# Optimization experiments

Measured on AMD Instinct MI355X. Metric: run time of the kernel, lower is better.

## Reference

```python
import jax, jax.numpy as jnp
import numpy as np

N, E, DIM = 50000, 500000, 64
EIN3, EIN4 = 16, 16

def setup_inputs() -> dict:
    key = jax.random.key(0)
    ks = jax.random.split(key, 8)
    x = jax.random.normal(ks[0], (N, DIM), dtype=jnp.float32)
    edge_index3 = jax.random.randint(ks[1], (2, E), 0, N, dtype=jnp.int64)
    edge_attr3 = jax.random.normal(ks[2], (E, EIN3), dtype=jnp.float32)
    edge_attr4 = jax.random.normal(ks[3], (E, EIN4), dtype=jnp.float32)
    batch = jnp.zeros((N,), dtype=jnp.int64)
    # MLP params: Linear(2*dim, 4*dim) -> ReLU -> Linear(4*dim, 1)
    W1 = jax.random.normal(ks[4], (2 * DIM, 4 * DIM), dtype=jnp.float32) / np.sqrt(2 * DIM)
    b1 = jnp.zeros((4 * DIM,), dtype=jnp.float32)
    W2 = jax.random.normal(ks[5], (4 * DIM, 1), dtype=jnp.float32) / np.sqrt(4 * DIM)
    b2 = jnp.zeros((1,), dtype=jnp.float32)
    return {"x": x, "edge_index3": edge_index3, "edge_attr3": edge_attr3,
            "edge_attr4": edge_attr4, "batch": batch,
            "W1": W1, "b1": b1, "W2": W2, "b2": b2}

def reference(x, edge_index3, edge_attr3, edge_attr4, batch, W1, b1, W2, b2):
    # gather endpoints: temp[k] = x[edge_index3[k]] -> [E, dim]
    src = x[edge_index3[0]]  # [E, dim]
    dst = x[edge_index3[1]]  # [E, dim]
    # symmetric concat: [[src|dst], [dst|src]] -> [2E, 2*dim]
    yhat = jnp.concatenate([
        jnp.concatenate([src, dst], axis=1),
        jnp.concatenate([dst, src], axis=1)], axis=0)
    h = jax.nn.relu(yhat @ W1 + b1)        # [2E, 4*dim]
    y = (h @ W2 + b2)[:, 0]                # [2E]
    return y.reshape(2, -1).mean(axis=0)   # [E]
```

## Files before the change

### kernel.cpp

```cpp
#include <hip/hip_runtime.h>

#define DIM 64
#define HID 256
#define ROWB 512
#define QSCALE  25.4f
#define DQSCALE (5.0f/127.0f)

typedef short s8v  __attribute__((ext_vector_type(8)));
typedef float f4v  __attribute__((ext_vector_type(4)));
typedef float f2v  __attribute__((ext_vector_type(2)));
typedef unsigned short u16x2 __attribute__((ext_vector_type(2)));

union U16 { uint4 u; s8v s; };

__device__ __forceinline__ unsigned short bf16_rne(float f) {
    unsigned u = __float_as_uint(f);
    u = (u + 0x7fffu + ((u >> 16) & 1u)) >> 16;
    return (unsigned short)u;
}
__device__ __forceinline__ unsigned pk_bf16(float a, float b) {
    return (unsigned)bf16_rne(a) | ((unsigned)bf16_rne(b) << 16);
}

__device__ __forceinline__ u16x2 as_u16x2(unsigned v) { union { unsigned u; u16x2 s; } c; c.u = v; return c.s; }
__device__ __forceinline__ unsigned as_u32(u16x2 v)   { union { u16x2 s; unsigned u; } c; c.s = v; return c.u; }

#define DPP_ADD(x, ctrl, rmask)                                               \
    (x) += __int_as_float(__builtin_amdgcn_update_dpp(                        \
        0, __float_as_int(x), (ctrl), (rmask), 0xf, true))
#define DPP_REDUCE5(x) do {                                                   \
    DPP_ADD(x, 0x111, 0xf);                                                   \
    DPP_ADD(x, 0x112, 0xf);                                                   \
    DPP_ADD(x, 0x114, 0xf);                                                   \
    DPP_ADD(x, 0x118, 0xf);                                                   \
    DPP_ADD(x, 0x142, 0xa);                                                   \
} while (0)

__global__ __launch_bounds__(256) void prep_wfrag(
    const float* __restrict__ W1, unsigned short* __restrict__ wf)
{
    const int f = blockIdx.x * 256 + threadIdx.x;
    if (f >= 32 * 2 * 64) return;
    const int lane = f & 63;
    const int t    = (f >> 6) & 1;
    const int ct   = f >> 7;
    const int col  = ct * 16 + (lane & 15);
    const int k0   = t * 32 + (lane >> 4) * 8;
    const float* __restrict__ wsrc =
        W1 + ((col >= HID) ? (DIM * HID + col - HID) : col);
    unsigned short v[8];
#pragma unroll
    for (int j = 0; j < 8; ++j) v[j] = bf16_rne(wsrc[(size_t)(k0 + j) * HID]);
    uint4 o;
    o.x = (unsigned)v[0] | ((unsigned)v[1] << 16);
    o.y = (unsigned)v[2] | ((unsigned)v[3] << 16);
    o.z = (unsigned)v[4] | ((unsigned)v[5] << 16);
    o.w = (unsigned)v[6] | ((unsigned)v[7] << 16);
    *(uint4*)(wf + (size_t)f * 8) = o;
}

__global__ __launch_bounds__(256) void node_mfma_q(
    const float* __restrict__ x, const unsigned short* __restrict__ wf,
    const float* __restrict__ b1, unsigned char* __restrict__ tab, int n)
{
    const int lane    = threadIdx.x & 63;
    const int w       = threadIdx.x >> 6;
    const int rowgrp  = w >> 1;
    const int colhalf = w & 1;
    const int m       = lane & 15;
    const int quad    = lane >> 4;
    const int rbase   = blockIdx.x * 32 + rowgrp * 16;

    const int arow = rbase + m;
    const float* __restrict__ xr = x + (size_t)((arow < n) ? arow : (n - 1)) * DIM;
    s8v a[2];
#pragma unroll
    for (int t = 0; t < 2; ++t) {
        const float4 lo = *(const float4*)(xr + t * 32 + quad * 8);
        const float4 hi = *(const float4*)(xr + t * 32 + quad * 8 + 4);
        U16 u;
        u.u.x = pk_bf16(lo.x, lo.y);
        u.u.y = pk_bf16(lo.z, lo.w);
        u.u.z = pk_bf16(hi.x, hi.y);
        u.u.w = pk_bf16(hi.z, hi.w);
        a[t] = u.s;
    }

    const uint4* __restrict__ wfv = (const uint4*)wf;

    f4v acc[16];
#pragma unroll
    for (int ct = 0; ct < 16; ++ct) {
        const int ctg = colhalf * 16 + ct;
        U16 b0u, b1u;
        b0u.u = wfv[(ctg * 2 + 0) * 64 + lane];
        b1u.u = wfv[(ctg * 2 + 1) * 64 + lane];
        f4v c = {0.f, 0.f, 0.f, 0.f};
        c = __builtin_amdgcn_mfma_f32_16x16x32_bf16(a[0], b0u.s, c, 0, 0, 0);
        c = __builtin_amdgcn_mfma_f32_16x16x32_bf16(a[1], b1u.s, c, 0, 0, 0);
        if (colhalf == 0) {
            const float bias = b1[ctg * 16 + m];
            c[0] += bias; c[1] += bias; c[2] += bias; c[3] += bias;
        }
        acc[ct] = c;
    }

#pragma unroll
    for (int r = 0; r < 4; ++r) {
        const int gr = rbase + quad * 4 + r;
        if (gr >= n) continue;
        unsigned b[16];
#pragma unroll
        for (int ct = 0; ct < 16; ++ct) {
            float v = __builtin_rintf(acc[ct][r] * QSCALE);
            v = fminf(fmaxf(v, -127.f), 127.f);
            b[ct] = (unsigned)((int)v + 127);
        }
        uint4 o;
        o.x = b[0]  | (b[1]  << 8) | (b[2]  << 16) | (b[3]  << 24);
        o.y = b[4]  | (b[5]  << 8) | (b[6]  << 16) | (b[7]  << 24);
        o.z = b[8]  | (b[9]  << 8) | (b[10] << 16) | (b[11] << 24);
        o.w = b[12] | (b[13] << 8) | (b[14] << 16) | (b[15] << 24);
        *(uint4*)(tab + (size_t)gr * ROWB + colhalf * 256 + m * 16) = o;
    }
}

__device__ __forceinline__ float pass_dot(const uint4 S, const uint4 D,
                                          const f2v* __restrict__ w)
{
    const unsigned sa[4] = {S.x, S.y, S.z, S.w};
    const unsigned da[4] = {D.x, D.y, D.z, D.w};
    const u16x2 k254 = {254, 254};
    f2v acc; acc.x = 0.f; acc.y = 0.f;
#pragma unroll
    for (int i = 0; i < 4; ++i) {
        const unsigned zs0 = __builtin_amdgcn_perm(0u, sa[i], 0x0C010C00u);
        const unsigned zs1 = __builtin_amdgcn_perm(0u, sa[i], 0x0C030C02u);
        const unsigned zd0 = __builtin_amdgcn_perm(0u, da[i], 0x0C010C00u);
        const unsigned zd1 = __builtin_amdgcn_perm(0u, da[i], 0x0C030C02u);
        const unsigned r0 = as_u32(__builtin_elementwise_sub_sat(
                                as_u16x2(zs0) + as_u16x2(zd0), k254));
        const unsigned r1 = as_u32(__builtin_elementwise_sub_sat(
                                as_u16x2(zs1) + as_u16x2(zd1), k254));
        f2v f0, f1;
        f0.x = (float)(r0 & 0xffu);
        f0.y = (float)((r0 >> 16) & 0xffu);
        f1.x = (float)(r1 & 0xffu);
        f1.y = (float)((r1 >> 16) & 0xffu);
        acc = f0 * w[2 * i] + acc;
        acc = f1 * w[2 * i + 1] + acc;
    }
    return acc.x + acc.y;
}

__global__ __launch_bounds__(256, 8) void edge_mlp_q(
    const int* __restrict__ ei, const unsigned char* __restrict__ tab,
    const float* __restrict__ W2, const float* __restrict__ b2,
    float* __restrict__ out, int ne)
{
    const int lane = threadIdx.x & 63;
    const int l31  = lane & 31;
    const int m    = lane & 15;
    const bool hi  = lane >= 32;

    f2v w[8];
#pragma unroll
    for (int i = 0; i < 4; ++i) {
        f2v w0, w1;
        w0.x = W2[(4 * i + 0) * 16 + m]; w0.y = W2[(4 * i + 1) * 16 + m];
        w1.x = W2[(4 * i + 2) * 16 + m]; w1.y = W2[(4 * i + 3) * 16 + m];
        w[2 * i] = w0; w[2 * i + 1] = w1;
    }
    const float bias = b2[0];
    const float sc   = 0.5f * DQSCALE;

    const unsigned offS = 16u * (unsigned)l31;
    const unsigned offD = 16u * (unsigned)(l31 ^ 16);

    const int wid = blockIdx.x * 4 + (threadIdx.x >> 6);
    const int nw  = (int)gridDim.x * 4;
    const int ne4 = ne & ~3;

    for (int e0 = wid * 4; e0 < ne4; e0 += nw * 4) {
        const int eu = __builtin_amdgcn_readfirstlane(e0);
        const int s0 = ei[eu],          s1 = ei[eu + 1];
        const int s2 = ei[eu + 2],      s3 = ei[eu + 3];
        const int d0 = ei[ne + eu],     d1 = ei[ne + eu + 1];
        const int d2 = ei[ne + eu + 2], d3 = ei[ne + eu + 3];

        const uint4 T0 = *(const uint4*)(tab + (((unsigned)(hi ? s1 : s0)) << 9) + offS);
        const uint4 T1 = *(const uint4*)(tab + (((unsigned)(hi ? d1 : d0)) << 9) + offD);
        const uint4 T2 = *(const uint4*)(tab + (((unsigned)(hi ? s3 : s2)) << 9) + offS);
        const uint4 T3 = *(const uint4*)(tab + (((unsigned)(hi ? d3 : d2)) << 9) + offD);

        float r0 = pass_dot(T0, T1, w);
        DPP_REDUCE5(r0);
        float r1 = pass_dot(T2, T3, w);
        DPP_REDUCE5(r1);

        if (l31 == 31) {
            const int eo = eu + (lane >> 5);
            out[eo]     = fmaf(sc, r0, bias);
            out[eo + 2] = fmaf(sc, r1, bias);
        }
    }

    if ((ne & 3) && wid == 0) {
        for (int e = ne4; e < ne; ++e) {
            const int s = ei[e], d = ei[ne + e];
            const uint4 S = *(const uint4*)(tab + ((unsigned)s << 9) + offS);
            const uint4 D = *(const uint4*)(tab + ((unsigned)d << 9) + offD);
            float r = pass_dot(S, D, w);
            DPP_REDUCE5(r);
            if (lane == 31) out[e] = fmaf(sc, r, bias);
        }
    }
}

extern "C" void kernel_launch(void* const* d_in, const int* in_sizes, int n_in,
                              void* d_out, int out_size, void* d_ws, size_t ws_size,
                              hipStream_t stream) {
    const float* x  = (const float*)d_in[0];
    const int*   ei = (const int*)d_in[1];
    const float* W1 = (const float*)d_in[5];
    const float* b1 = (const float*)d_in[6];
    const float* W2 = (const float*)d_in[7];
    const float* b2 = (const float*)d_in[8];
    float* out = (float*)d_out;

    const int n  = in_sizes[0] / DIM;
    const int ne = in_sizes[1] / 2;

    unsigned char*  tab = (unsigned char*)d_ws;
    unsigned short* wf  = (unsigned short*)(tab + (size_t)n * ROWB);

    prep_wfrag<<<16, 256, 0, stream>>>(W1, wf);
    node_mfma_q<<<(n + 31) / 32, 256, 0, stream>>>(x, wf, b1, tab, n);
    edge_mlp_q<<<8192, 256, 0, stream>>>(ei, tab, W2, b2, out, ne);
}
```

Baseline: 187.3 us.

## Process one edge per full wave with 8-byte loads and 64-lane reduction

Each edge is now spread across all 64 lanes, with each lane loading 8 bytes instead of 16 from the precomputed quantized table. Before, each 32-lane half-wave handled a different edge. The wave issues 8 gathers for 4 edges and reduces each with a 6-step DPP sum across 64 lanes. One lane writes the 4 outputs as a single float4 store. The aim is smaller per-lane loads, fewer VGPRs and a vectorized store, at the cost of more cross-lane reduction steps and more load instructions.

New measurement: 186.6 us. About the same (-0.4%).

```diff
diff --git a/kernel.cpp b/kernel.cpp
--- a/kernel.cpp
+++ b/kernel.cpp
@@ -28,12 +28,13 @@
 #define DPP_ADD(x, ctrl, rmask)                                               \
     (x) += __int_as_float(__builtin_amdgcn_update_dpp(                        \
         0, __float_as_int(x), (ctrl), (rmask), 0xf, true))
-#define DPP_REDUCE5(x) do {                                                   \
-    DPP_ADD(x, 0x111, 0xf);                                                   \
-    DPP_ADD(x, 0x112, 0xf);                                                   \
-    DPP_ADD(x, 0x114, 0xf);                                                   \
-    DPP_ADD(x, 0x118, 0xf);                                                   \
-    DPP_ADD(x, 0x142, 0xa);                                                   \
+#define WAVE_SUM64(x) do {                                                    \
+    DPP_ADD(x, 0x111, 0xf);                                   \
+    DPP_ADD(x, 0x112, 0xf);                                   \
+    DPP_ADD(x, 0x114, 0xf);                                   \
+    DPP_ADD(x, 0x118, 0xf);                                   \
+    DPP_ADD(x, 0x142, 0xa);                                 \
+    DPP_ADD(x, 0x143, 0xc);               \
 } while (0)
 
 __global__ __launch_bounds__(256) void prep_wfrag(
@@ -125,31 +126,33 @@
     }
 }
 
-__device__ __forceinline__ float pass_dot(const uint4 S, const uint4 D,
+__device__ __forceinline__ void dot_dword(const unsigned s, const unsigned d,
+                                          const f2v wlo, const f2v whi, f2v& acc)
+{
+    const u16x2 k254 = {254, 254};
+    const unsigned zs0 = __builtin_amdgcn_perm(0u, s, 0x0C010C00u);
+    const unsigned zs1 = __builtin_amdgcn_perm(0u, s, 0x0C030C02u);
+    const unsigned zd0 = __builtin_amdgcn_perm(0u, d, 0x0C010C00u);
+    const unsigned zd1 = __builtin_amdgcn_perm(0u, d, 0x0C030C02u);
+    const unsigned r0 = as_u32(__builtin_elementwise_sub_sat(
+                            as_u16x2(zs0) + as_u16x2(zd0), k254));
+    const unsigned r1 = as_u32(__builtin_elementwise_sub_sat(
+                            as_u16x2(zs1) + as_u16x2(zd1), k254));
+    f2v f0, f1;
+    f0.x = (float)(r0 & 0xffu);
+    f0.y = (float)((r0 >> 16) & 0xffu);
+    f1.x = (float)(r1 & 0xffu);
+    f1.y = (float)((r1 >> 16) & 0xffu);
+    acc = f0 * wlo + acc;
+    acc = f1 * whi + acc;
+}
+
+__device__ __forceinline__ float pair_dot(const uint2 S, const uint2 D,
                                           const f2v* __restrict__ w)
 {
-    const unsigned sa[4] = {S.x, S.y, S.z, S.w};
-    const unsigned da[4] = {D.x, D.y, D.z, D.w};
-    const u16x2 k254 = {254, 254};
     f2v acc; acc.x = 0.f; acc.y = 0.f;
-#pragma unroll
-    for (int i = 0; i < 4; ++i) {
-        const unsigned zs0 = __builtin_amdgcn_perm(0u, sa[i], 0x0C010C00u);
-        const unsigned zs1 = __builtin_amdgcn_perm(0u, sa[i], 0x0C030C02u);
-        const unsigned zd0 = __builtin_amdgcn_perm(0u, da[i], 0x0C010C00u);
-        const unsigned zd1 = __builtin_amdgcn_perm(0u, da[i], 0x0C030C02u);
-        const unsigned r0 = as_u32(__builtin_elementwise_sub_sat(
-                                as_u16x2(zs0) + as_u16x2(zd0), k254));
-        const unsigned r1 = as_u32(__builtin_elementwise_sub_sat(
-                                as_u16x2(zs1) + as_u16x2(zd1), k254));
-        f2v f0, f1;
-        f0.x = (float)(r0 & 0xffu);
-        f0.y = (float)((r0 >> 16) & 0xffu);
-        f1.x = (float)(r1 & 0xffu);
-        f1.y = (float)((r1 >> 16) & 0xffu);
-        acc = f0 * w[2 * i] + acc;
-        acc = f1 * w[2 * i + 1] + acc;
-    }
+    dot_dword(S.x, D.x, w[0], w[1], acc);
+    dot_dword(S.y, D.y, w[2], w[3], acc);
     return acc.x + acc.y;
 }
 
@@ -159,23 +162,23 @@
     float* __restrict__ out, int ne)
 {
     const int lane = threadIdx.x & 63;
-    const int l31  = lane & 31;
-    const int m    = lane & 15;
-    const bool hi  = lane >= 32;
-
-    f2v w[8];
-#pragma unroll
-    for (int i = 0; i < 4; ++i) {
-        f2v w0, w1;
-        w0.x = W2[(4 * i + 0) * 16 + m]; w0.y = W2[(4 * i + 1) * 16 + m];
-        w1.x = W2[(4 * i + 2) * 16 + m]; w1.y = W2[(4 * i + 3) * 16 + m];
-        w[2 * i] = w0; w[2 * i + 1] = w1;
+    const int lp   = lane & 31;
+    const int mcol = lp >> 1;
+    const int ctb  = (lp & 1) * 8;
+
+    f2v w[4];
+#pragma unroll
+    for (int k = 0; k < 4; ++k) {
+        f2v t;
+        t.x = W2[(ctb + 2 * k)     * 16 + mcol];
+        t.y = W2[(ctb + 2 * k + 1) * 16 + mcol];
+        w[k] = t;
     }
     const float bias = b2[0];
     const float sc   = 0.5f * DQSCALE;
 
-    const unsigned offS = 16u * (unsigned)l31;
-    const unsigned offD = 16u * (unsigned)(l31 ^ 16);
+    const unsigned offS = 8u * (unsigned)lane;
+    const unsigned offD = 8u * (unsigned)(lane ^ 32);
 
     const int wid = blockIdx.x * 4 + (threadIdx.x >> 6);
     const int nw  = (int)gridDim.x * 4;
@@ -183,36 +186,36 @@
 
     for (int e0 = wid * 4; e0 < ne4; e0 += nw * 4) {
         const int eu = __builtin_amdgcn_readfirstlane(e0);
-        const int s0 = ei[eu],          s1 = ei[eu + 1];
-        const int s2 = ei[eu + 2],      s3 = ei[eu + 3];
-        const int d0 = ei[ne + eu],     d1 = ei[ne + eu + 1];
-        const int d2 = ei[ne + eu + 2], d3 = ei[ne + eu + 3];
-
-        const uint4 T0 = *(const uint4*)(tab + (((unsigned)(hi ? s1 : s0)) << 9) + offS);
-        const uint4 T1 = *(const uint4*)(tab + (((unsigned)(hi ? d1 : d0)) << 9) + offD);
-        const uint4 T2 = *(const uint4*)(tab + (((unsigned)(hi ? s3 : s2)) << 9) + offS);
-        const uint4 T3 = *(const uint4*)(tab + (((unsigned)(hi ? d3 : d2)) << 9) + offD);
-
-        float r0 = pass_dot(T0, T1, w);
-        DPP_REDUCE5(r0);
-        float r1 = pass_dot(T2, T3, w);
-        DPP_REDUCE5(r1);
-
-        if (l31 == 31) {
-            const int eo = eu + (lane >> 5);
-            out[eo]     = fmaf(sc, r0, bias);
-            out[eo + 2] = fmaf(sc, r1, bias);
+        uint2 hs[4], hd[4];
+#pragma unroll
+        for (int q = 0; q < 4; ++q) {
+            const int s = ei[eu + q];
+            const int d = ei[ne + eu + q];
+            hs[q] = *(const uint2*)(tab + ((size_t)(unsigned)s << 9) + offS);
+            hd[q] = *(const uint2*)(tab + ((size_t)(unsigned)d << 9) + offD);
+        }
+        float r[4];
+#pragma unroll
+        for (int q = 0; q < 4; ++q) {
+            float s = pair_dot(hs[q], hd[q], w);
+            WAVE_SUM64(s);
+            r[q] = s;
+        }
+        if (lane == 63) {
+            *(float4*)(out + eu) = make_float4(
+                fmaf(sc, r[0], bias), fmaf(sc, r[1], bias),
+                fmaf(sc, r[2], bias), fmaf(sc, r[3], bias));
         }
     }
 
     if ((ne & 3) && wid == 0) {
         for (int e = ne4; e < ne; ++e) {
             const int s = ei[e], d = ei[ne + e];
-            const uint4 S = *(const uint4*)(tab + ((unsigned)s << 9) + offS);
-            const uint4 D = *(const uint4*)(tab + ((unsigned)d << 9) + offD);
-            float r = pass_dot(S, D, w);
-            DPP_REDUCE5(r);
-            if (lane == 31) out[e] = fmaf(sc, r, bias);
+            const uint2 S = *(const uint2*)(tab + ((size_t)(unsigned)s << 9) + offS);
+            const uint2 D = *(const uint2*)(tab + ((size_t)(unsigned)d << 9) + offD);
+            float r = pair_dot(S, D, w);
+            WAVE_SUM64(r);
+            if (lane == 63) out[e] = fmaf(sc, r, bias);
         }
     }
 }
```
